# Kernel tuning notes

Measured on AMD Instinct MI355X. Metric: run time of the kernel, lower is better.

## Reference

```python
import jax, jax.numpy as jnp
import numpy as np

N, G, C, A, E = 10000, 12, 64, 3, 50000
LN_EPS = 1e-5


def setup_inputs() -> dict:
    key = jax.random.key(0)
    ks = jax.random.split(key, 12)
    s = 0.05
    return {
        "x": jax.random.normal(ks[0], (N, G, C), jnp.float32),
        "edge_attr": jax.random.normal(ks[1], (E, G, G, A), jnp.float32),
        "W_kernel": jax.random.normal(ks[2], (A, C), jnp.float32) * s,   # depthwise kernel basis Linear(attr_dim->C)
        "conv_bias": jax.random.normal(ks[3], (C,), jnp.float32) * s,
        "ln_w": jnp.ones((C,), jnp.float32),
        "ln_b": jnp.zeros((C,), jnp.float32),
        "W1": jax.random.normal(ks[4], (C, C), jnp.float32) * s,          # stored [in,out]
        "b1": jax.random.normal(ks[5], (C,), jnp.float32) * s,
        "W2": jax.random.normal(ks[6], (C, C), jnp.float32) * s,
        "b2": jax.random.normal(ks[7], (C,), jnp.float32) * s,
        "layer_scale": jnp.full((1, C), 1e-6, jnp.float32),
        "edge_index": jax.random.randint(ks[8], (2, E), 0, N, jnp.int32),
        "batch": jnp.zeros((N,), jnp.int32),
    }


def reference(x, edge_attr, W_kernel, conv_bias, ln_w, ln_b, W1, b1, W2, b2,
              layer_scale, edge_index, batch):
    src, dst = edge_index[0], edge_index[1]
    x_j = x[src]                                            # [E,G,C] gather
    # depthwise fiber conv: m[e,g,c] = sum_{h,a} attr[e,g,h,a] * Wk[a,c] * x_j[e,h,c]
    # contract over source grid h first to avoid materializing the [E,G,G,C] kernel
    t = jnp.einsum('egha,ehc->egac', edge_attr, x_j)        # [E,G,A,C]
    m = jnp.einsum('egac,ac->egc', t, W_kernel)             # [E,G,C]
    agg = jnp.zeros_like(x).at[dst].add(m) + conv_bias      # scatter-add, [N,G,C]
    # LayerNorm over channel dim
    mu = jnp.mean(agg, axis=-1, keepdims=True)
    var = jnp.mean(jnp.square(agg - mu), axis=-1, keepdims=True)
    h = (agg - mu) * jax.lax.rsqrt(var + LN_EPS) * ln_w + ln_b
    # 2-layer MLP with exact GELU (torch default)
    h = jax.nn.gelu(h @ W1 + b1, approximate=False) @ W2 + b2
    h = layer_scale * h                                     # broadcast [1,C] over [N,G,C]
    return x + h                                            # residual (same shape)
```

## Files before the change

### kernel.cpp

```cpp
#include <hip/hip_runtime.h>
#include <math.h>

#define NN 10000
#define GG 12
#define CC 64
#define AA 3
#define EE 50000
#define LN_EPS 1e-5f
#define MAXDEG 64

typedef __attribute__((ext_vector_type(4))) float f4;
typedef __attribute__((ext_vector_type(4))) short s4;

union S4U { s4 s; unsigned int w[2]; };
union I2S { int i[2]; s4 s; };

__device__ __forceinline__ s4 pack4(float k0, float k1, float k2, float k3) {
    S4U t;
    t.w[0] = __builtin_amdgcn_perm(__float_as_uint(k1), __float_as_uint(k0), 0x07060302u);
    t.w[1] = __builtin_amdgcn_perm(__float_as_uint(k3), __float_as_uint(k2), 0x07060302u);
    return t.s;
}
__device__ __forceinline__ unsigned int pack2(float a, float b) {
    return __builtin_amdgcn_perm(__float_as_uint(b), __float_as_uint(a), 0x07060302u);
}

__device__ __forceinline__ f4 mfma_bf16(s4 a, s4 b, f4 c) {
#if __has_builtin(__builtin_amdgcn_mfma_f32_16x16x16bf16_1k)
    return __builtin_amdgcn_mfma_f32_16x16x16bf16_1k(a, b, c, 0, 0, 0);
#else
    asm volatile("v_mfma_f32_16x16x16_bf16 %0, %1, %2, %0" : "+v"(c) : "v"(a), "v"(b));
    return c;
#endif
}

__global__ __launch_bounds__(256) void zero_cnt(int* __restrict__ cnt) {
    int i = blockIdx.x * 256 + threadIdx.x;
    if (i < NN) cnt[i] = 0;
}

__global__ __launch_bounds__(256) void bucket_fill(const int* __restrict__ ei,
                                                   int* __restrict__ cnt,
                                                   int* __restrict__ elist) {
    int e = blockIdx.x * 256 + threadIdx.x;
    if (e < EE) {
        int src = ei[e];
        int dst = ei[EE + e];
        int pos = atomicAdd(&cnt[dst], 1);
        if (pos < MAXDEG) elist[dst * MAXDEG + pos] = e | (src << 17);
    }
}

__global__ __launch_bounds__(256) void xpack(const float* __restrict__ x,
                                             unsigned int* __restrict__ xp) {
    const int l  = threadIdx.x & 63;
    const int n  = blockIdx.x * 4 + (threadIdx.x >> 6);
    const int lm = l & 15;
    const int lg = l >> 4;

    unsigned int d[8];
    if (lg < 3) {
        const char* xb = (const char*)(x + n * (GG * CC)) + lg * 1024 + lm * 4;
#pragma unroll
        for (int t = 0; t < 4; ++t) {
            const float v0 = *(const float*)(xb + t * 64 + 0 * 256);
            const float v1 = *(const float*)(xb + t * 64 + 1 * 256);
            const float v2 = *(const float*)(xb + t * 64 + 2 * 256);
            const float v3 = *(const float*)(xb + t * 64 + 3 * 256);
            d[2 * t]     = pack2(v0, v1);
            d[2 * t + 1] = pack2(v2, v3);
        }
    } else {
#pragma unroll
        for (int k = 0; k < 8; ++k) d[k] = 0u;
    }
    unsigned int* o = xp + (size_t)n * 512 + l * 8;
    *(uint4*)o       = make_uint4(d[0], d[1], d[2], d[3]);
    *(uint4*)(o + 4) = make_uint4(d[4], d[5], d[6], d[7]);
}

__global__ __launch_bounds__(64) void conv_mfma(
    const unsigned int* __restrict__ xp, const float* __restrict__ attr,
    const float* __restrict__ Wk,
    const int* __restrict__ cnt, const int* __restrict__ elist,
    float* __restrict__ agg) {
    __shared__ float lsa[2][432];

    const int l  = threadIdx.x;
    const int n  = blockIdx.x;
    const int lm = l & 15;
    const int lg = l >> 4;

    const int fbase = (lm < 12 && lg < 3) ? (lm * 36 + lg * 12) : 0;
    const int a1l   = (l < 44) ? l : 43;

    const int deg = min(cnt[n], MAXDEG);
    const int myE = elist[n * MAXDEG + l];

    f4 acc[3][4];
#pragma unroll
    for (int a = 0; a < 3; ++a)
#pragma unroll
        for (int t = 0; t < 4; ++t) acc[a][t] = (f4){0.f, 0.f, 0.f, 0.f};

    f4 Aa0, Aa1, Ab0, Ab1;
    int4 Xa0, Xa1, Xb0, Xb1;

#define LOADE(idx, A0, A1, X0, X1)                                              \
    {                                                                           \
        const int p = __builtin_amdgcn_readlane(myE, (idx));                    \
        const char* ab = (const char*)(attr + (size_t)(p & 0x1FFFF) * 432);     \
        A0 = *(const f4*)(ab + 16 * l);                                         \
        A1 = *(const f4*)(ab + 1024 + 16 * a1l);                                \
        const int* xb = (const int*)(xp + (size_t)(p >> 17) * 512 + 8 * l);     \
        X0 = *(const int4*)xb;                                                  \
        X1 = *(const int4*)(xb + 4);                                            \
    }

#define STAGE(slot, A0, A1)                                                     \
    {                                                                           \
        float* sw = &lsa[slot][0];                                              \
        *(f4*)(sw + 4 * l) = A0;                                                \
        if (l < 44) *(f4*)(sw + 256 + 4 * l) = A1;                              \
    }

#define COMPUTE(slot, X0, X1)                                                   \
    {                                                                           \
        I2S u0, u1, u2, u3;                                                     \
        u0.i[0] = X0.x; u0.i[1] = X0.y;                                         \
        u1.i[0] = X0.z; u1.i[1] = X0.w;                                         \
        u2.i[0] = X1.x; u2.i[1] = X1.y;                                         \
        u3.i[0] = X1.z; u3.i[1] = X1.w;                                         \
        const float* sr = &lsa[slot][0] + fbase;                                \
        const f4 q0 = *(const f4*)(sr);                                         \
        const f4 q1 = *(const f4*)(sr + 4);                                     \
        const f4 q2 = *(const f4*)(sr + 8);                                     \
        const s4 af0 = pack4(q0[0], q0[3], q1[2], q2[1]);                       \
        const s4 af1 = pack4(q0[1], q1[0], q1[3], q2[2]);                       \
        const s4 af2 = pack4(q0[2], q1[1], q2[0], q2[3]);                       \
        acc[0][0] = mfma_bf16(af0, u0.s, acc[0][0]);                            \
        acc[1][0] = mfma_bf16(af1, u0.s, acc[1][0]);                            \
        acc[2][0] = mfma_bf16(af2, u0.s, acc[2][0]);                            \
        acc[0][1] = mfma_bf16(af0, u1.s, acc[0][1]);                            \
        acc[1][1] = mfma_bf16(af1, u1.s, acc[1][1]);                            \
        acc[2][1] = mfma_bf16(af2, u1.s, acc[2][1]);                            \
        acc[0][2] = mfma_bf16(af0, u2.s, acc[0][2]);                            \
        acc[1][2] = mfma_bf16(af1, u2.s, acc[1][2]);                            \
        acc[2][2] = mfma_bf16(af2, u2.s, acc[2][2]);                            \
        acc[0][3] = mfma_bf16(af0, u3.s, acc[0][3]);                            \
        acc[1][3] = mfma_bf16(af1, u3.s, acc[1][3]);                            \
        acc[2][3] = mfma_bf16(af2, u3.s, acc[2][3]);                            \
    }

    if (deg > 0) LOADE(0, Aa0, Aa1, Xa0, Xa1);
    if (deg > 1) LOADE(1, Ab0, Ab1, Xb0, Xb1);
    if (deg > 0) STAGE(0, Aa0, Aa1);

    for (int i = 0; i < deg; i += 2) {
        if (i + 2 < deg) LOADE(i + 2, Aa0, Aa1, Xa0, Xa1);
        COMPUTE(0, Xa0, Xa1);
        if (i + 1 < deg) STAGE(1, Ab0, Ab1);

        if (i + 1 < deg) {
            COMPUTE(1, Xb0, Xb1);
            if (i + 3 < deg) LOADE(i + 3, Ab0, Ab1, Xb0, Xb1);
            if (i + 2 < deg) STAGE(0, Aa0, Aa1);
        }
    }

#undef LOADE
#undef STAGE
#undef COMPUTE

    float wk[3][4];
#pragma unroll
    for (int a = 0; a < 3; ++a)
#pragma unroll
        for (int t = 0; t < 4; ++t)
            wk[a][t] = Wk[a * CC + lm + 16 * t];

    float* ob = agg + (size_t)n * (GG * CC);
    if (lg < 3) {
#pragma unroll
        for (int t = 0; t < 4; ++t) {
#pragma unroll
            for (int r = 0; r < 4; ++r) {
                const float m = fmaf(acc[0][t][r], wk[0][t],
                                fmaf(acc[1][t][r], wk[1][t],
                                     acc[2][t][r] * wk[2][t]));
                ob[(lg * 4 + r) * CC + lm + 16 * t] = m;
            }
        }
    }
}

__global__ __launch_bounds__(256) void ln_mlp_mfma(
    const float* __restrict__ x, const float* __restrict__ cb,
    const float* __restrict__ lnw, const float* __restrict__ lnb,
    const float* __restrict__ W1, const float* __restrict__ b1,
    const float* __restrict__ W2, const float* __restrict__ b2,
    const float* __restrict__ ls, float* __restrict__ out) {
    __shared__ float sbuf[4][16 * 68];

    const int l  = threadIdx.x & 63;
    const int wv = threadIdx.x >> 6;
    const int lm = l & 15;
    const int lg = l >> 4;
    const int f0 = (blockIdx.x * 4 + wv) * 16;

    const float* aggp = out + (size_t)(f0 + lm) * CC + 4 * lg;
    f4 h4[4];
#pragma unroll
    for (int kt = 0; kt < 4; ++kt) h4[kt] = *(const f4*)(aggp + 16 * kt);

    f4 cb4[4], lw4[4], lb4[4];
#pragma unroll
    for (int kt = 0; kt < 4; ++kt) {
        cb4[kt] = *(const f4*)(cb  + 4 * lg + 16 * kt);
        lw4[kt] = *(const f4*)(lnw + 4 * lg + 16 * kt);
        lb4[kt] = *(const f4*)(lnb + 4 * lg + 16 * kt);
    }

    float s = 0.f, s2 = 0.f;
#pragma unroll
    for (int kt = 0; kt < 4; ++kt)
#pragma unroll
        for (int j = 0; j < 4; ++j) {
            const float v = h4[kt][j] + cb4[kt][j];
            h4[kt][j] = v;
            s += v; s2 += v * v;
        }
    s  += __shfl_xor(s, 16);  s  += __shfl_xor(s, 32);
    s2 += __shfl_xor(s2, 16); s2 += __shfl_xor(s2, 32);
    const float mu  = s * (1.f / 64.f);
    const float inv = rsqrtf(s2 * (1.f / 64.f) - mu * mu + LN_EPS);

    s4 hf[4];
#pragma unroll
    for (int kt = 0; kt < 4; ++kt) {
        const float n0 = (h4[kt][0] - mu) * inv * lw4[kt][0] + lb4[kt][0];
        const float n1 = (h4[kt][1] - mu) * inv * lw4[kt][1] + lb4[kt][1];
        const float n2 = (h4[kt][2] - mu) * inv * lw4[kt][2] + lb4[kt][2];
        const float n3 = (h4[kt][3] - mu) * inv * lw4[kt][3] + lb4[kt][3];
        hf[kt] = pack4(n0, n1, n2, n3);
    }

    s4 w1f[4][4];
#pragma unroll
    for (int mt = 0; mt < 4; ++mt)
#pragma unroll
        for (int kt = 0; kt < 4; ++kt) {
            const int kb = 4 * lg + 16 * kt;
            const int m  = lm + 16 * mt;
            w1f[mt][kt] = pack4(W1[(kb + 0) * CC + m], W1[(kb + 1) * CC + m],
                                W1[(kb + 2) * CC + m], W1[(kb + 3) * CC + m]);
        }

    f4 z[4];
#pragma unroll
    for (int mt = 0; mt < 4; ++mt) z[mt] = (f4){0.f, 0.f, 0.f, 0.f};
#pragma unroll
    for (int mt = 0; mt < 4; ++mt)
#pragma unroll
        for (int kt = 0; kt < 4; ++kt)
            z[mt] = mfma_bf16(w1f[mt][kt], hf[kt], z[mt]);

    s4 gf[4];
#pragma unroll
    for (int mt = 0; mt < 4; ++mt) {
        const f4 b14 = *(const f4*)(b1 + 16 * mt + 4 * lg);
        float g[4];
#pragma unroll
        for (int r = 0; r < 4; ++r) {
            const float zz = z[mt][r] + b14[r];
            g[r] = 0.5f * zz * (1.f + erff(zz * 0.70710678118654752f));
        }
        gf[mt] = pack4(g[0], g[1], g[2], g[3]);
    }

    s4 w2f[4][4];
#pragma unroll
    for (int mt = 0; mt < 4; ++mt)
#pragma unroll
        for (int kt = 0; kt < 4; ++kt) {
            const int kb = 4 * lg + 16 * kt;
            const int m  = lm + 16 * mt;
            w2f[mt][kt] = pack4(W2[(kb + 0) * CC + m], W2[(kb + 1) * CC + m],
                                W2[(kb + 2) * CC + m], W2[(kb + 3) * CC + m]);
        }

    f4 o[4];
#pragma unroll
    for (int mt = 0; mt < 4; ++mt) o[mt] = (f4){0.f, 0.f, 0.f, 0.f};
#pragma unroll
    for (int mt = 0; mt < 4; ++mt)
#pragma unroll
        for (int kt = 0; kt < 4; ++kt)
            o[mt] = mfma_bf16(w2f[mt][kt], gf[kt], o[mt]);

    float* sb = sbuf[wv];
    const int fbase = lm * 68;
    const int swz   = (l & 7) << 2;
#pragma unroll
    for (int mt = 0; mt < 4; ++mt)
#pragma unroll
        for (int r = 0; r < 4; ++r)
            sb[fbase + ((16 * mt + 4 * lg + r) ^ swz)] = o[mt][r];

    const f4 b2q = *(const f4*)(b2 + 4 * lm);
    const f4 lsq = *(const f4*)(ls + 4 * lm);

#pragma unroll
    for (int rr = 0; rr < 4; ++rr) {
        const int R   = rr * 4 + lg;
        const int col = 4 * lm;
        const f4 ov = *(const f4*)(&sb[R * 68 + (col ^ ((R & 7) << 2))]);
        const f4 xv = *(const f4*)(x + (size_t)(f0 + R) * CC + col);
        f4 res;
#pragma unroll
        for (int k = 0; k < 4; ++k)
            res[k] = fmaf(lsq[k], ov[k] + b2q[k], xv[k]);
        *(f4*)(out + (size_t)(f0 + R) * CC + col) = res;
    }
}

extern "C" void kernel_launch(void* const* d_in, const int* in_sizes, int n_in,
                              void* d_out, int out_size, void* d_ws, size_t ws_size,
                              hipStream_t stream) {
    const float* x    = (const float*)d_in[0];
    const float* attr = (const float*)d_in[1];
    const float* Wk   = (const float*)d_in[2];
    const float* cb   = (const float*)d_in[3];
    const float* lnw  = (const float*)d_in[4];
    const float* lnb  = (const float*)d_in[5];
    const float* W1   = (const float*)d_in[6];
    const float* b1   = (const float*)d_in[7];
    const float* W2   = (const float*)d_in[8];
    const float* b2   = (const float*)d_in[9];
    const float* ls   = (const float*)d_in[10];
    const int*   ei   = (const int*)d_in[11];
    float* out = (float*)d_out;

    int* cnt   = (int*)d_ws;
    int* elist = cnt + NN;
    unsigned int* xp = (unsigned int*)(elist + NN * MAXDEG);

    zero_cnt<<<(NN + 255) / 256, 256, 0, stream>>>(cnt);
    bucket_fill<<<(EE + 255) / 256, 256, 0, stream>>>(ei, cnt, elist);
    xpack<<<NN / 4, 256, 0, stream>>>(x, xp);
    conv_mfma<<<NN, 64, 0, stream>>>(xp, attr, Wk, cnt, elist, out);
    ln_mlp_mfma<<<1875, 256, 0, stream>>>(x, cb, lnw, lnb, W1, b1, W2, b2, ls, out);
}
```

Before: 79.32 us.

## Split each node's edge loop across two waves and fuse count zeroing into xpack

The conv kernel now runs 256-thread blocks that cover two nodes, with two waves per node. Each wave handles alternate edges, and the two partial results are summed through shared memory before the store. The goal is to halve the serial latency of the per-node gather-and-MFMA chain and to keep more waves in flight. The count-zeroing kernel is merged into xpack, removing one launch. The cost is more LDS use and a block-wide barrier, and each wave has less work to hide load latency behind.

```diff
diff --git a/kernel.cpp b/kernel.cpp
--- a/kernel.cpp
+++ b/kernel.cpp
@@ -34,9 +34,36 @@
 #endif
 }
 
-__global__ __launch_bounds__(256) void zero_cnt(int* __restrict__ cnt) {
-    int i = blockIdx.x * 256 + threadIdx.x;
-    if (i < NN) cnt[i] = 0;
+__global__ __launch_bounds__(256) void xpack(const float* __restrict__ x,
+                                             unsigned int* __restrict__ xp,
+                                             int* __restrict__ cnt) {
+    const int gid = blockIdx.x * 256 + threadIdx.x;
+    if (gid < NN) cnt[gid] = 0;
+
+    const int l  = threadIdx.x & 63;
+    const int n  = blockIdx.x * 4 + (threadIdx.x >> 6);
+    const int lm = l & 15;
+    const int lg = l >> 4;
+
+    unsigned int d[8];
+    if (lg < 3) {
+        const char* xb = (const char*)(x + n * (GG * CC)) + lg * 1024 + lm * 4;
+#pragma unroll
+        for (int t = 0; t < 4; ++t) {
+            const float v0 = *(const float*)(xb + t * 64 + 0 * 256);
+            const float v1 = *(const float*)(xb + t * 64 + 1 * 256);
+            const float v2 = *(const float*)(xb + t * 64 + 2 * 256);
+            const float v3 = *(const float*)(xb + t * 64 + 3 * 256);
+            d[2 * t]     = pack2(v0, v1);
+            d[2 * t + 1] = pack2(v2, v3);
+        }
+    } else {
+#pragma unroll
+        for (int k = 0; k < 8; ++k) d[k] = 0u;
+    }
+    unsigned int* o = xp + (size_t)n * 512 + l * 8;
+    *(uint4*)o       = make_uint4(d[0], d[1], d[2], d[3]);
+    *(uint4*)(o + 4) = make_uint4(d[4], d[5], d[6], d[7]);
 }
 
 __global__ __launch_bounds__(256) void bucket_fill(const int* __restrict__ ei,
@@ -51,51 +78,28 @@
     }
 }
 
-__global__ __launch_bounds__(256) void xpack(const float* __restrict__ x,
-                                             unsigned int* __restrict__ xp) {
-    const int l  = threadIdx.x & 63;
-    const int n  = blockIdx.x * 4 + (threadIdx.x >> 6);
-    const int lm = l & 15;
-    const int lg = l >> 4;
-
-    unsigned int d[8];
-    if (lg < 3) {
-        const char* xb = (const char*)(x + n * (GG * CC)) + lg * 1024 + lm * 4;
-#pragma unroll
-        for (int t = 0; t < 4; ++t) {
-            const float v0 = *(const float*)(xb + t * 64 + 0 * 256);
-            const float v1 = *(const float*)(xb + t * 64 + 1 * 256);
-            const float v2 = *(const float*)(xb + t * 64 + 2 * 256);
-            const float v3 = *(const float*)(xb + t * 64 + 3 * 256);
-            d[2 * t]     = pack2(v0, v1);
-            d[2 * t + 1] = pack2(v2, v3);
-        }
-    } else {
-#pragma unroll
-        for (int k = 0; k < 8; ++k) d[k] = 0u;
-    }
-    unsigned int* o = xp + (size_t)n * 512 + l * 8;
-    *(uint4*)o       = make_uint4(d[0], d[1], d[2], d[3]);
-    *(uint4*)(o + 4) = make_uint4(d[4], d[5], d[6], d[7]);
-}
-
-__global__ __launch_bounds__(64) void conv_mfma(
+__global__ __launch_bounds__(256) void conv_mfma(
     const unsigned int* __restrict__ xp, const float* __restrict__ attr,
     const float* __restrict__ Wk,
     const int* __restrict__ cnt, const int* __restrict__ elist,
     float* __restrict__ agg) {
-    __shared__ float lsa[2][432];
-
-    const int l  = threadIdx.x;
-    const int n  = blockIdx.x;
-    const int lm = l & 15;
-    const int lg = l >> 4;
+    __shared__ float lsa[4][2][432];
+    __shared__ float red[2][768];
+
+    const int l   = threadIdx.x & 63;
+    const int w   = threadIdx.x >> 6;
+    const int sub = w & 1;
+    const int par = w >> 1;
+    const int n   = blockIdx.x * 2 + sub;
+    const int lm  = l & 15;
+    const int lg  = l >> 4;
 
     const int fbase = (lm < 12 && lg < 3) ? (lm * 36 + lg * 12) : 0;
     const int a1l   = (l < 44) ? l : 43;
 
     const int deg = min(cnt[n], MAXDEG);
     const int myE = elist[n * MAXDEG + l];
+    const int m   = (deg > par) ? ((deg - par + 1) >> 1) : 0;
 
     f4 acc[3][4];
 #pragma unroll
@@ -119,7 +123,7 @@
 
 #define STAGE(slot, A0, A1)                                                     \
     {                                                                           \
-        float* sw = &lsa[slot][0];                                              \
+        float* sw = &lsa[w][slot][0];                                           \
         *(f4*)(sw + 4 * l) = A0;                                                \
         if (l < 44) *(f4*)(sw + 256 + 4 * l) = A1;                              \
     }
@@ -131,7 +135,7 @@
         u1.i[0] = X0.z; u1.i[1] = X0.w;                                         \
         u2.i[0] = X1.x; u2.i[1] = X1.y;                                         \
         u3.i[0] = X1.z; u3.i[1] = X1.w;                                         \
-        const float* sr = &lsa[slot][0] + fbase;                                \
+        const float* sr = &lsa[w][slot][0] + fbase;                             \
         const f4 q0 = *(const f4*)(sr);                                         \
         const f4 q1 = *(const f4*)(sr + 4);                                     \
         const f4 q2 = *(const f4*)(sr + 8);                                     \
@@ -152,19 +156,18 @@
         acc[2][3] = mfma_bf16(af2, u3.s, acc[2][3]);                            \
     }
 
-    if (deg > 0) LOADE(0, Aa0, Aa1, Xa0, Xa1);
-    if (deg > 1) LOADE(1, Ab0, Ab1, Xb0, Xb1);
-    if (deg > 0) STAGE(0, Aa0, Aa1);
-
-    for (int i = 0; i < deg; i += 2) {
-        if (i + 2 < deg) LOADE(i + 2, Aa0, Aa1, Xa0, Xa1);
+    if (m > 0) LOADE(par, Aa0, Aa1, Xa0, Xa1);
+    if (m > 1) LOADE(par + 2, Ab0, Ab1, Xb0, Xb1);
+    if (m > 0) STAGE(0, Aa0, Aa1);
+
+    for (int j = 0; j < m; j += 2) {
         COMPUTE(0, Xa0, Xa1);
-        if (i + 1 < deg) STAGE(1, Ab0, Ab1);
-
-        if (i + 1 < deg) {
+        if (j + 2 < m) LOADE(par + 2 * (j + 2), Aa0, Aa1, Xa0, Xa1);
+        if (j + 1 < m) {
+            STAGE(1, Ab0, Ab1);
             COMPUTE(1, Xb0, Xb1);
-            if (i + 3 < deg) LOADE(i + 3, Ab0, Ab1, Xb0, Xb1);
-            if (i + 2 < deg) STAGE(0, Aa0, Aa1);
+            if (j + 3 < m) LOADE(par + 2 * (j + 3), Ab0, Ab1, Xb0, Xb1);
+            if (j + 2 < m) STAGE(0, Aa0, Aa1);
         }
     }
 
@@ -179,18 +182,30 @@
         for (int t = 0; t < 4; ++t)
             wk[a][t] = Wk[a * CC + lm + 16 * t];
 
-    float* ob = agg + (size_t)n * (GG * CC);
-    if (lg < 3) {
-#pragma unroll
-        for (int t = 0; t < 4; ++t) {
+    float mval[16];
+#pragma unroll
+    for (int t = 0; t < 4; ++t)
+#pragma unroll
+        for (int r = 0; r < 4; ++r)
+            mval[4 * t + r] = fmaf(acc[0][t][r], wk[0][t],
+                               fmaf(acc[1][t][r], wk[1][t],
+                                    acc[2][t][r] * wk[2][t]));
+
+    if (par == 1 && l < 48) {
+#pragma unroll
+        for (int idx = 0; idx < 16; ++idx)
+            red[sub][idx * 48 + l] = mval[idx];
+    }
+    __syncthreads();
+    if (par == 0 && l < 48) {
+        float* ob = agg + (size_t)n * (GG * CC);
+#pragma unroll
+        for (int t = 0; t < 4; ++t)
 #pragma unroll
             for (int r = 0; r < 4; ++r) {
-                const float m = fmaf(acc[0][t][r], wk[0][t],
-                                fmaf(acc[1][t][r], wk[1][t],
-                                     acc[2][t][r] * wk[2][t]));
-                ob[(lg * 4 + r) * CC + lm + 16 * t] = m;
+                const float v = mval[4 * t + r] + red[sub][(4 * t + r) * 48 + l];
+                ob[(lg * 4 + r) * CC + lm + 16 * t] = v;
             }
-        }
     }
 }
 
@@ -345,9 +360,8 @@
     int* elist = cnt + NN;
     unsigned int* xp = (unsigned int*)(elist + NN * MAXDEG);
 
-    zero_cnt<<<(NN + 255) / 256, 256, 0, stream>>>(cnt);
+    xpack<<<NN / 4, 256, 0, stream>>>(x, xp, cnt);
     bucket_fill<<<(EE + 255) / 256, 256, 0, stream>>>(ei, cnt, elist);
-    xpack<<<NN / 4, 256, 0, stream>>>(x, xp);
-    conv_mfma<<<NN, 64, 0, stream>>>(xp, attr, Wk, cnt, elist, out);
+    conv_mfma<<<NN / 2, 256, 0, stream>>>(xp, attr, Wk, cnt, elist, out);
     ln_mlp_mfma<<<1875, 256, 0, stream>>>(x, cb, lnw, lnb, W1, b1, W2, b2, ls, out);
 }
```

New measurement: 74.85 us. 5.6% less time.

## Deepen conv edge prefetch to four, pack four nodes per block, fuse zeroing

Applied to the files above, without the earlier changes.

The conv kernel now keeps four edges' attribute and feature loads in flight instead of two, clamping out-of-range indices so loads are issued unconditionally. Each block now handles four nodes (one wave each) with per-wave LDS buffers instead of one wave per block. The count-zeroing kernel is merged into xpack, which removes one launch. Together these aim to hide gather latency and cut launch and block-scheduling overhead, at the cost of more registers and redundant loads for low-degree nodes.

```diff
diff --git a/kernel.cpp b/kernel.cpp
--- a/kernel.cpp
+++ b/kernel.cpp
@@ -34,9 +34,36 @@
 #endif
 }
 
-__global__ __launch_bounds__(256) void zero_cnt(int* __restrict__ cnt) {
-    int i = blockIdx.x * 256 + threadIdx.x;
-    if (i < NN) cnt[i] = 0;
+__global__ __launch_bounds__(256) void xpack(const float* __restrict__ x,
+                                             unsigned int* __restrict__ xp,
+                                             int* __restrict__ cnt) {
+    const int gid = blockIdx.x * 256 + threadIdx.x;
+    if (gid < NN) cnt[gid] = 0;
+
+    const int l  = threadIdx.x & 63;
+    const int n  = blockIdx.x * 4 + (threadIdx.x >> 6);
+    const int lm = l & 15;
+    const int lg = l >> 4;
+
+    unsigned int d[8];
+    if (lg < 3) {
+        const char* xb = (const char*)(x + n * (GG * CC)) + lg * 1024 + lm * 4;
+#pragma unroll
+        for (int t = 0; t < 4; ++t) {
+            const float v0 = *(const float*)(xb + t * 64 + 0 * 256);
+            const float v1 = *(const float*)(xb + t * 64 + 1 * 256);
+            const float v2 = *(const float*)(xb + t * 64 + 2 * 256);
+            const float v3 = *(const float*)(xb + t * 64 + 3 * 256);
+            d[2 * t]     = pack2(v0, v1);
+            d[2 * t + 1] = pack2(v2, v3);
+        }
+    } else {
+#pragma unroll
+        for (int k = 0; k < 8; ++k) d[k] = 0u;
+    }
+    unsigned int* o = xp + (size_t)n * 512 + l * 8;
+    *(uint4*)o       = make_uint4(d[0], d[1], d[2], d[3]);
+    *(uint4*)(o + 4) = make_uint4(d[4], d[5], d[6], d[7]);
 }
 
 __global__ __launch_bounds__(256) void bucket_fill(const int* __restrict__ ei,
@@ -51,43 +78,16 @@
     }
 }
 
-__global__ __launch_bounds__(256) void xpack(const float* __restrict__ x,
-                                             unsigned int* __restrict__ xp) {
-    const int l  = threadIdx.x & 63;
-    const int n  = blockIdx.x * 4 + (threadIdx.x >> 6);
-    const int lm = l & 15;
-    const int lg = l >> 4;
-
-    unsigned int d[8];
-    if (lg < 3) {
-        const char* xb = (const char*)(x + n * (GG * CC)) + lg * 1024 + lm * 4;
-#pragma unroll
-        for (int t = 0; t < 4; ++t) {
-            const float v0 = *(const float*)(xb + t * 64 + 0 * 256);
-            const float v1 = *(const float*)(xb + t * 64 + 1 * 256);
-            const float v2 = *(const float*)(xb + t * 64 + 2 * 256);
-            const float v3 = *(const float*)(xb + t * 64 + 3 * 256);
-            d[2 * t]     = pack2(v0, v1);
-            d[2 * t + 1] = pack2(v2, v3);
-        }
-    } else {
-#pragma unroll
-        for (int k = 0; k < 8; ++k) d[k] = 0u;
-    }
-    unsigned int* o = xp + (size_t)n * 512 + l * 8;
-    *(uint4*)o       = make_uint4(d[0], d[1], d[2], d[3]);
-    *(uint4*)(o + 4) = make_uint4(d[4], d[5], d[6], d[7]);
-}
-
-__global__ __launch_bounds__(64) void conv_mfma(
+__global__ __launch_bounds__(256) void conv_mfma(
     const unsigned int* __restrict__ xp, const float* __restrict__ attr,
     const float* __restrict__ Wk,
     const int* __restrict__ cnt, const int* __restrict__ elist,
     float* __restrict__ agg) {
-    __shared__ float lsa[2][432];
-
-    const int l  = threadIdx.x;
-    const int n  = blockIdx.x;
+    __shared__ float lsa[4][2][432];
+
+    const int l  = threadIdx.x & 63;
+    const int w  = threadIdx.x >> 6;
+    const int n  = blockIdx.x * 4 + w;
     const int lm = l & 15;
     const int lg = l >> 4;
 
@@ -103,12 +103,13 @@
 #pragma unroll
         for (int t = 0; t < 4; ++t) acc[a][t] = (f4){0.f, 0.f, 0.f, 0.f};
 
-    f4 Aa0, Aa1, Ab0, Ab1;
-    int4 Xa0, Xa1, Xb0, Xb1;
+    f4 Aa0, Aa1, Ab0, Ab1, Ac0, Ac1, Ad0, Ad1;
+    int4 Xa0, Xa1, Xb0, Xb1, Xc0, Xc1, Xd0, Xd1;
 
 #define LOADE(idx, A0, A1, X0, X1)                                              \
     {                                                                           \
-        const int p = __builtin_amdgcn_readlane(myE, (idx));                    \
+        const int ic = ((idx) < deg) ? (idx) : (deg - 1);                       \
+        const int p = __builtin_amdgcn_readlane(myE, ic);                       \
         const char* ab = (const char*)(attr + (size_t)(p & 0x1FFFF) * 432);     \
         A0 = *(const f4*)(ab + 16 * l);                                         \
         A1 = *(const f4*)(ab + 1024 + 16 * a1l);                                \
@@ -119,7 +120,7 @@
 
 #define STAGE(slot, A0, A1)                                                     \
     {                                                                           \
-        float* sw = &lsa[slot][0];                                              \
+        float* sw = &lsa[w][slot][0];                                           \
         *(f4*)(sw + 4 * l) = A0;                                                \
         if (l < 44) *(f4*)(sw + 256 + 4 * l) = A1;                              \
     }
@@ -131,7 +132,7 @@
         u1.i[0] = X0.z; u1.i[1] = X0.w;                                         \
         u2.i[0] = X1.x; u2.i[1] = X1.y;                                         \
         u3.i[0] = X1.z; u3.i[1] = X1.w;                                         \
-        const float* sr = &lsa[slot][0] + fbase;                                \
+        const float* sr = &lsa[w][slot][0] + fbase;                             \
         const f4 q0 = *(const f4*)(sr);                                         \
         const f4 q1 = *(const f4*)(sr + 4);                                     \
         const f4 q2 = *(const f4*)(sr + 8);                                     \
@@ -152,19 +153,33 @@
         acc[2][3] = mfma_bf16(af2, u3.s, acc[2][3]);                            \
     }
 
-    if (deg > 0) LOADE(0, Aa0, Aa1, Xa0, Xa1);
-    if (deg > 1) LOADE(1, Ab0, Ab1, Xb0, Xb1);
-    if (deg > 0) STAGE(0, Aa0, Aa1);
-
-    for (int i = 0; i < deg; i += 2) {
-        if (i + 2 < deg) LOADE(i + 2, Aa0, Aa1, Xa0, Xa1);
-        COMPUTE(0, Xa0, Xa1);
-        if (i + 1 < deg) STAGE(1, Ab0, Ab1);
-
-        if (i + 1 < deg) {
-            COMPUTE(1, Xb0, Xb1);
-            if (i + 3 < deg) LOADE(i + 3, Ab0, Ab1, Xb0, Xb1);
-            if (i + 2 < deg) STAGE(0, Aa0, Aa1);
+    if (deg > 0) {
+        LOADE(0, Aa0, Aa1, Xa0, Xa1);
+        LOADE(1, Ab0, Ab1, Xb0, Xb1);
+        LOADE(2, Ac0, Ac1, Xc0, Xc1);
+        LOADE(3, Ad0, Ad1, Xd0, Xd1);
+        STAGE(0, Aa0, Aa1);
+        if (deg > 1) STAGE(1, Ab0, Ab1);
+
+        for (int i = 0; i < deg; i += 4) {
+            COMPUTE(0, Xa0, Xa1);
+            if (i + 2 < deg) STAGE(0, Ac0, Ac1);
+            LOADE(i + 4, Aa0, Aa1, Xa0, Xa1);
+            if (i + 1 < deg) {
+                COMPUTE(1, Xb0, Xb1);
+                if (i + 3 < deg) STAGE(1, Ad0, Ad1);
+                LOADE(i + 5, Ab0, Ab1, Xb0, Xb1);
+                if (i + 2 < deg) {
+                    COMPUTE(0, Xc0, Xc1);
+                    if (i + 4 < deg) STAGE(0, Aa0, Aa1);
+                    LOADE(i + 6, Ac0, Ac1, Xc0, Xc1);
+                    if (i + 3 < deg) {
+                        COMPUTE(1, Xd0, Xd1);
+                        if (i + 5 < deg) STAGE(1, Ab0, Ab1);
+                        LOADE(i + 7, Ad0, Ad1, Xd0, Xd1);
+                    }
+                }
+            }
         }
     }
 
@@ -345,9 +360,8 @@
     int* elist = cnt + NN;
     unsigned int* xp = (unsigned int*)(elist + NN * MAXDEG);
 
-    zero_cnt<<<(NN + 255) / 256, 256, 0, stream>>>(cnt);
+    xpack<<<NN / 4, 256, 0, stream>>>(x, xp, cnt);
     bucket_fill<<<(EE + 255) / 256, 256, 0, stream>>>(ei, cnt, elist);
-    xpack<<<NN / 4, 256, 0, stream>>>(x, xp);
-    conv_mfma<<<NN, 64, 0, stream>>>(xp, attr, Wk, cnt, elist, out);
+    conv_mfma<<<NN / 4, 256, 0, stream>>>(xp, attr, Wk, cnt, elist, out);
     ln_mlp_mfma<<<1875, 256, 0, stream>>>(x, cb, lnw, lnb, W1, b1, W2, b2, ls, out);
 }
```

Measured after the change: 78.31 us. About the same (-1.3%).

## Fuse count zeroing into xpack and make conv kernel persistent with 8 waves

Applied to the files above, without the earlier changes.

Zeroing of the degree counters is folded into the xpack kernel, which removes one launch. The conv kernel becomes a grid-stride persistent kernel with 8 waves per block, each wave owning a node and its own LDS double buffer, and Wk is hoisted out of the per-node loop. The pipeline order inside the edge loop is slightly reordered. The LN/MLP kernel moves to 512-thread blocks with a bounds guard. The aim is to cut launch and block-scheduling overhead, at the risk of lower occupancy from the larger LDS footprint and load imbalance across nodes of different degree.

```diff
diff --git a/kernel.cpp b/kernel.cpp
--- a/kernel.cpp
+++ b/kernel.cpp
@@ -34,9 +34,36 @@
 #endif
 }
 
-__global__ __launch_bounds__(256) void zero_cnt(int* __restrict__ cnt) {
-    int i = blockIdx.x * 256 + threadIdx.x;
-    if (i < NN) cnt[i] = 0;
+__global__ __launch_bounds__(256) void xpack(const float* __restrict__ x,
+                                             unsigned int* __restrict__ xp,
+                                             int* __restrict__ cnt) {
+    const int gid = blockIdx.x * 256 + threadIdx.x;
+    if (gid < NN) cnt[gid] = 0;
+
+    const int l  = threadIdx.x & 63;
+    const int n  = blockIdx.x * 4 + (threadIdx.x >> 6);
+    const int lm = l & 15;
+    const int lg = l >> 4;
+
+    unsigned int d[8];
+    if (lg < 3) {
+        const char* xb = (const char*)(x + n * (GG * CC)) + lg * 1024 + lm * 4;
+#pragma unroll
+        for (int t = 0; t < 4; ++t) {
+            const float v0 = *(const float*)(xb + t * 64 + 0 * 256);
+            const float v1 = *(const float*)(xb + t * 64 + 1 * 256);
+            const float v2 = *(const float*)(xb + t * 64 + 2 * 256);
+            const float v3 = *(const float*)(xb + t * 64 + 3 * 256);
+            d[2 * t]     = pack2(v0, v1);
+            d[2 * t + 1] = pack2(v2, v3);
+        }
+    } else {
+#pragma unroll
+        for (int k = 0; k < 8; ++k) d[k] = 0u;
+    }
+    unsigned int* o = xp + (size_t)n * 512 + l * 8;
+    *(uint4*)o       = make_uint4(d[0], d[1], d[2], d[3]);
+    *(uint4*)(o + 4) = make_uint4(d[4], d[5], d[6], d[7]);
 }
 
 __global__ __launch_bounds__(256) void bucket_fill(const int* __restrict__ ei,
@@ -51,60 +78,40 @@
     }
 }
 
-__global__ __launch_bounds__(256) void xpack(const float* __restrict__ x,
-                                             unsigned int* __restrict__ xp) {
-    const int l  = threadIdx.x & 63;
-    const int n  = blockIdx.x * 4 + (threadIdx.x >> 6);
-    const int lm = l & 15;
-    const int lg = l >> 4;
-
-    unsigned int d[8];
-    if (lg < 3) {
-        const char* xb = (const char*)(x + n * (GG * CC)) + lg * 1024 + lm * 4;
-#pragma unroll
-        for (int t = 0; t < 4; ++t) {
-            const float v0 = *(const float*)(xb + t * 64 + 0 * 256);
-            const float v1 = *(const float*)(xb + t * 64 + 1 * 256);
-            const float v2 = *(const float*)(xb + t * 64 + 2 * 256);
-            const float v3 = *(const float*)(xb + t * 64 + 3 * 256);
-            d[2 * t]     = pack2(v0, v1);
-            d[2 * t + 1] = pack2(v2, v3);
-        }
-    } else {
-#pragma unroll
-        for (int k = 0; k < 8; ++k) d[k] = 0u;
-    }
-    unsigned int* o = xp + (size_t)n * 512 + l * 8;
-    *(uint4*)o       = make_uint4(d[0], d[1], d[2], d[3]);
-    *(uint4*)(o + 4) = make_uint4(d[4], d[5], d[6], d[7]);
-}
-
-__global__ __launch_bounds__(64) void conv_mfma(
+__global__ __launch_bounds__(512) void conv_mfma(
     const unsigned int* __restrict__ xp, const float* __restrict__ attr,
     const float* __restrict__ Wk,
     const int* __restrict__ cnt, const int* __restrict__ elist,
     float* __restrict__ agg) {
-    __shared__ float lsa[2][432];
-
-    const int l  = threadIdx.x;
-    const int n  = blockIdx.x;
+    __shared__ float lsa[8][2][432];
+
+    const int l  = threadIdx.x & 63;
+    const int w  = threadIdx.x >> 6;
     const int lm = l & 15;
     const int lg = l >> 4;
 
     const int fbase = (lm < 12 && lg < 3) ? (lm * 36 + lg * 12) : 0;
     const int a1l   = (l < 44) ? l : 43;
 
-    const int deg = min(cnt[n], MAXDEG);
-    const int myE = elist[n * MAXDEG + l];
-
-    f4 acc[3][4];
+    float wk[3][4];
 #pragma unroll
     for (int a = 0; a < 3; ++a)
 #pragma unroll
-        for (int t = 0; t < 4; ++t) acc[a][t] = (f4){0.f, 0.f, 0.f, 0.f};
-
-    f4 Aa0, Aa1, Ab0, Ab1;
-    int4 Xa0, Xa1, Xb0, Xb1;
+        for (int t = 0; t < 4; ++t)
+            wk[a][t] = Wk[a * CC + lm + 16 * t];
+
+    for (int n = blockIdx.x * 8 + w; n < NN; n += gridDim.x * 8) {
+        const int deg = min(cnt[n], MAXDEG);
+        const int myE = elist[n * MAXDEG + l];
+
+        f4 acc[3][4];
+#pragma unroll
+        for (int a = 0; a < 3; ++a)
+#pragma unroll
+            for (int t = 0; t < 4; ++t) acc[a][t] = (f4){0.f, 0.f, 0.f, 0.f};
+
+        f4 Aa0, Aa1, Ab0, Ab1;
+        int4 Xa0, Xa1, Xb0, Xb1;
 
 #define LOADE(idx, A0, A1, X0, X1)                                              \
     {                                                                           \
@@ -119,7 +126,7 @@
 
 #define STAGE(slot, A0, A1)                                                     \
     {                                                                           \
-        float* sw = &lsa[slot][0];                                              \
+        float* sw = &lsa[w][slot][0];                                           \
         *(f4*)(sw + 4 * l) = A0;                                                \
         if (l < 44) *(f4*)(sw + 256 + 4 * l) = A1;                              \
     }
@@ -131,7 +138,7 @@
         u1.i[0] = X0.z; u1.i[1] = X0.w;                                         \
         u2.i[0] = X1.x; u2.i[1] = X1.y;                                         \
         u3.i[0] = X1.z; u3.i[1] = X1.w;                                         \
-        const float* sr = &lsa[slot][0] + fbase;                                \
+        const float* sr = &lsa[w][slot][0] + fbase;                             \
         const f4 q0 = *(const f4*)(sr);                                         \
         const f4 q1 = *(const f4*)(sr + 4);                                     \
         const f4 q2 = *(const f4*)(sr + 8);                                     \
@@ -152,61 +159,55 @@
         acc[2][3] = mfma_bf16(af2, u3.s, acc[2][3]);                            \
     }
 
-    if (deg > 0) LOADE(0, Aa0, Aa1, Xa0, Xa1);
-    if (deg > 1) LOADE(1, Ab0, Ab1, Xb0, Xb1);
-    if (deg > 0) STAGE(0, Aa0, Aa1);
-
-    for (int i = 0; i < deg; i += 2) {
-        if (i + 2 < deg) LOADE(i + 2, Aa0, Aa1, Xa0, Xa1);
-        COMPUTE(0, Xa0, Xa1);
-        if (i + 1 < deg) STAGE(1, Ab0, Ab1);
-
-        if (i + 1 < deg) {
-            COMPUTE(1, Xb0, Xb1);
-            if (i + 3 < deg) LOADE(i + 3, Ab0, Ab1, Xb0, Xb1);
-            if (i + 2 < deg) STAGE(0, Aa0, Aa1);
-        }
-    }
+        if (deg > 0) LOADE(0, Aa0, Aa1, Xa0, Xa1);
+        if (deg > 1) LOADE(1, Ab0, Ab1, Xb0, Xb1);
+        if (deg > 0) STAGE(0, Aa0, Aa1);
+
+        for (int j = 0; j < deg; j += 2) {
+            COMPUTE(0, Xa0, Xa1);
+            if (j + 2 < deg) LOADE(j + 2, Aa0, Aa1, Xa0, Xa1);
+            if (j + 1 < deg) {
+                STAGE(1, Ab0, Ab1);
+                COMPUTE(1, Xb0, Xb1);
+                if (j + 3 < deg) LOADE(j + 3, Ab0, Ab1, Xb0, Xb1);
+                if (j + 2 < deg) STAGE(0, Aa0, Aa1);
+            }
+        }
 
 #undef LOADE
 #undef STAGE
 #undef COMPUTE
 
-    float wk[3][4];
-#pragma unroll
-    for (int a = 0; a < 3; ++a)
-#pragma unroll
-        for (int t = 0; t < 4; ++t)
-            wk[a][t] = Wk[a * CC + lm + 16 * t];
-
-    float* ob = agg + (size_t)n * (GG * CC);
-    if (lg < 3) {
-#pragma unroll
-        for (int t = 0; t < 4; ++t) {
-#pragma unroll
-            for (int r = 0; r < 4; ++r) {
-                const float m = fmaf(acc[0][t][r], wk[0][t],
-                                fmaf(acc[1][t][r], wk[1][t],
-                                     acc[2][t][r] * wk[2][t]));
-                ob[(lg * 4 + r) * CC + lm + 16 * t] = m;
+        float* ob = agg + (size_t)n * (GG * CC);
+        if (lg < 3) {
+#pragma unroll
+            for (int t = 0; t < 4; ++t) {
+#pragma unroll
+                for (int r = 0; r < 4; ++r) {
+                    const float m = fmaf(acc[0][t][r], wk[0][t],
+                                    fmaf(acc[1][t][r], wk[1][t],
+                                         acc[2][t][r] * wk[2][t]));
+                    ob[(lg * 4 + r) * CC + lm + 16 * t] = m;
+                }
             }
         }
     }
 }
 
-__global__ __launch_bounds__(256) void ln_mlp_mfma(
+__global__ __launch_bounds__(512) void ln_mlp_mfma(
     const float* __restrict__ x, const float* __restrict__ cb,
     const float* __restrict__ lnw, const float* __restrict__ lnb,
     const float* __restrict__ W1, const float* __restrict__ b1,
     const float* __restrict__ W2, const float* __restrict__ b2,
     const float* __restrict__ ls, float* __restrict__ out) {
-    __shared__ float sbuf[4][16 * 68];
+    __shared__ float sbuf[8][16 * 68];
 
     const int l  = threadIdx.x & 63;
     const int wv = threadIdx.x >> 6;
     const int lm = l & 15;
     const int lg = l >> 4;
-    const int f0 = (blockIdx.x * 4 + wv) * 16;
+    const int f0 = (blockIdx.x * 8 + wv) * 16;
+    if (f0 >= NN * GG) return;
 
     const float* aggp = out + (size_t)(f0 + lm) * CC + 4 * lg;
     f4 h4[4];
@@ -345,9 +346,8 @@
     int* elist = cnt + NN;
     unsigned int* xp = (unsigned int*)(elist + NN * MAXDEG);
 
-    zero_cnt<<<(NN + 255) / 256, 256, 0, stream>>>(cnt);
+    xpack<<<NN / 4, 256, 0, stream>>>(x, xp, cnt);
     bucket_fill<<<(EE + 255) / 256, 256, 0, stream>>>(ei, cnt, elist);
-    xpack<<<NN / 4, 256, 0, stream>>>(x, xp);
-    conv_mfma<<<NN, 64, 0, stream>>>(xp, attr, Wk, cnt, elist, out);
-    ln_mlp_mfma<<<1875, 256, 0, stream>>>(x, cb, lnw, lnb, W1, b1, W2, b2, ls, out);
-}
+    conv_mfma<<<640, 512, 0, stream>>>(xp, attr, Wk, cnt, elist, out);
+    ln_mlp_mfma<<<938, 512, 0, stream>>>(x, cb, lnw, lnb, W1, b1, W2, b2, ls, out);
+}
```

After: 76.63 us. 1.04x faster.
